# Kernel optimization log

Hardware: AMD Instinct MI355X
Metric: run time of the kernel (lower is better)

The kernel has to match this reference:

```python
import jax, jax.numpy as jnp
import numpy as np

N = 50000
E = 800000
D_IN = 128
D_OUT = 128


def setup_inputs() -> dict:
    key = jax.random.key(0)
    ks = jax.random.split(key, 12)
    x = jax.random.normal(ks[0], (N, D_IN), dtype=jnp.float32)
    W1 = jax.random.normal(ks[1], (D_IN, D_OUT), dtype=jnp.float32) * (1.0 / np.sqrt(D_IN))
    b1 = jnp.zeros((D_OUT,), dtype=jnp.float32)
    W2 = jax.random.normal(ks[2], (D_IN, D_OUT), dtype=jnp.float32) * (1.0 / np.sqrt(D_IN))
    b2 = jnp.zeros((D_OUT,), dtype=jnp.float32)
    # inverted-dropout masks, p=0.5 -> values in {0, 2}
    def mask(k):
        return jnp.where(jax.random.uniform(k, (N, D_IN)) < 0.5, 0.0, 2.0).astype(jnp.float32)
    mask_pos1 = mask(ks[3])
    mask_neg1 = mask(ks[4])
    mask_pos2 = mask(ks[5])
    mask_neg2 = mask(ks[6])
    edge_index1 = jax.random.randint(ks[7], (2, E), 0, N, dtype=jnp.int32)
    edge_index2 = jax.random.randint(ks[8], (2, E), 0, N, dtype=jnp.int32)
    perm1 = jax.random.permutation(ks[9], N).astype(jnp.int32)
    perm2 = jax.random.permutation(ks[10], N).astype(jnp.int32)
    return dict(x=x, W1=W1, b1=b1, W2=W2, b2=b2,
                mask_pos1=mask_pos1, mask_neg1=mask_neg1,
                mask_pos2=mask_pos2, mask_neg2=mask_neg2,
                edge_index1=edge_index1, edge_index2=edge_index2,
                perm1=perm1, perm2=perm2)


def gcn_conv(x, W, b, edge_index):
    """PyG GCNConv: add self-loops, symmetric normalization, then x@W aggregation + bias."""
    n = x.shape[0]
    xw = x @ W  # [N, D_OUT]
    loops = jnp.arange(n, dtype=edge_index.dtype)
    src = jnp.concatenate([edge_index[0], loops])
    dst = jnp.concatenate([edge_index[1], loops])
    deg = jax.ops.segment_sum(jnp.ones_like(dst, dtype=xw.dtype), dst, num_segments=n)
    dinv = jax.lax.rsqrt(jnp.maximum(deg, 1.0))  # deg >= 1 due to self-loops
    norm = dinv[src] * dinv[dst]                 # [E+N]
    msg = xw[src] * norm[:, None]                # [E+N, D_OUT]
    out = jax.ops.segment_sum(msg, dst, num_segments=n)
    return out + b


def _branch(x, W, b, edge_index, mask_pos, mask_neg, perm):
    pos_h = jax.nn.relu(gcn_conv(x * mask_pos, W, b, edge_index))
    neg_in = (x * mask_neg)[perm]
    neg_h = jax.nn.relu(gcn_conv(neg_in, W, b, edge_index))
    summary = jnp.mean(pos_h, axis=0, keepdims=True)  # [1, D_OUT]
    return pos_h, neg_h, summary


def reference(x, W1, b1, W2, b2, mask_pos1, mask_neg1, mask_pos2, mask_neg2,
              edge_index1, edge_index2, perm1, perm2):
    p1, n1, s1 = _branch(x, W1, b1, edge_index1, mask_pos1, mask_neg1, perm1)
    p2, n2, s2 = _branch(x, W2, b2, edge_index2, mask_pos2, mask_neg2, perm2)
    return (p1, n1, s1, p2, n2, s2)
```

## Files before the change

kernel.cpp:

```cpp
#include <hip/hip_runtime.h>
#include <hip/hip_fp16.h>

#define NN 50000
#define NE 800000
#define D 128
#define NB 196
#define FILL_BLOCKS 1024
#define GEMM_BLOCKS 3128
#define RNG 6250
#define ESL 6250

typedef _Float16 half8_t __attribute__((ext_vector_type(8)));
typedef _Float16 half4_t __attribute__((ext_vector_type(4)));
typedef float f32x4 __attribute__((ext_vector_type(4)));

__global__ void k_init(int* cnt1, int* cnt2, float* s1, float* s2) {
    int i = blockIdx.x * blockDim.x + threadIdx.x;
    int stride = gridDim.x * blockDim.x;
    for (int j = i; j < NN; j += stride) { cnt1[j] = 0; cnt2[j] = 0; }
    if (i < D) { s1[i] = 0.f; s2[i] = 0.f; }
}

__global__ void k_count(const int* __restrict__ dst1, const int* __restrict__ dst2,
                        int* cnt1, int* cnt2) {
    int r = blockIdx.x & 7;
    int rank = blockIdx.x >> 3;
    unsigned lo = r * RNG;
    int base = rank * ESL;
    for (int e = base + threadIdx.x; e < base + ESL; e += 256) {
        int d1 = dst1[e];
        if ((unsigned)(d1 - lo) < RNG) atomicAdd(&cnt1[d1], 1);
        int d2 = dst2[e];
        if ((unsigned)(d2 - lo) < RNG) atomicAdd(&cnt2[d2], 1);
    }
}

__global__ void k_part(const int* __restrict__ cnt1, const int* __restrict__ cnt2,
                       int* part1, int* part2) {
    __shared__ int sm1[256], sm2[256];
    int t = threadIdx.x;
    int idx = blockIdx.x * 256 + t;
    int v1 = (idx < NN) ? cnt1[idx] : 0;
    int v2 = (idx < NN) ? cnt2[idx] : 0;
    sm1[t] = v1; sm2[t] = v2;
    __syncthreads();
    for (int off = 128; off > 0; off >>= 1) {
        if (t < off) { sm1[t] += sm1[t + off]; sm2[t] += sm2[t + off]; }
        __syncthreads();
    }
    if (t == 0) { part1[blockIdx.x] = sm1[0]; part2[blockIdx.x] = sm2[0]; }
}

__global__ void k_scanp(int* part1, int* part2) {
    __shared__ int sm1[256], sm2[256];
    int t = threadIdx.x;
    int v1 = (t < NB) ? part1[t] : 0;
    int v2 = (t < NB) ? part2[t] : 0;
    sm1[t] = v1; sm2[t] = v2;
    __syncthreads();
    for (int off = 1; off < 256; off <<= 1) {
        int a1 = (t >= off) ? sm1[t - off] : 0;
        int a2 = (t >= off) ? sm2[t - off] : 0;
        __syncthreads();
        sm1[t] += a1; sm2[t] += a2;
        __syncthreads();
    }
    if (t < NB) { part1[t] = sm1[t] - v1; part2[t] = sm2[t] - v2; }
}

__global__ void k_apply(const int* __restrict__ cnt1, const int* __restrict__ cnt2,
                        const int* __restrict__ part1, const int* __restrict__ part2,
                        int* rp1, int* rp2, int* cur1, int* cur2,
                        float* dinv1, float* dinv2) {
    __shared__ int sm1[256], sm2[256];
    int b = blockIdx.x, t = threadIdx.x;
    int idx = b * 256 + t;
    int v1 = (idx < NN) ? cnt1[idx] : 0;
    int v2 = (idx < NN) ? cnt2[idx] : 0;
    sm1[t] = v1; sm2[t] = v2;
    __syncthreads();
    for (int off = 1; off < 256; off <<= 1) {
        int a1 = (t >= off) ? sm1[t - off] : 0;
        int a2 = (t >= off) ? sm2[t - off] : 0;
        __syncthreads();
        sm1[t] += a1; sm2[t] += a2;
        __syncthreads();
    }
    int e1 = sm1[t] - v1 + part1[b];
    int e2 = sm2[t] - v2 + part2[b];
    if (idx < NN) {
        rp1[idx] = e1; cur1[idx] = e1; dinv1[idx] = rsqrtf((float)(v1 + 1));
        rp2[idx] = e2; cur2[idx] = e2; dinv2[idx] = rsqrtf((float)(v2 + 1));
    } else if (idx == NN) {
        rp1[NN] = e1; rp2[NN] = e2;
    }
}

__launch_bounds__(256)
__global__ void k_fill_gemm(const int* __restrict__ src1, const int* __restrict__ dst1,
                            const int* __restrict__ src2, const int* __restrict__ dst2,
                            int* cur1, int* cur2, int* col1, int* col2,
                            const float* __restrict__ x,
                            const float* __restrict__ W1, const float* __restrict__ W2,
                            const float* __restrict__ mp1, const float* __restrict__ mn1,
                            const float* __restrict__ mp2, const float* __restrict__ mn2,
                            const int* __restrict__ perm1, const int* __restrict__ perm2,
                            const float* __restrict__ dinv1, const float* __restrict__ dinv2,
                            _Float16* xwi1, _Float16* xwi2) {
    __shared__ __align__(16) _Float16 WT[128][136];
    int t = threadIdx.x;
    int bid = blockIdx.x;

    if (bid < FILL_BLOCKS) {
        int r = bid & 7;
        int rank = bid >> 3;
        unsigned lo = r * RNG;
        int base = rank * ESL;
        for (int e = base + t; e < base + ESL; e += 256) {
            int d1 = dst1[e];
            if ((unsigned)(d1 - lo) < RNG) {
                int p = atomicAdd(&cur1[d1], 1);
                col1[p] = src1[e];
            }
            int d2 = dst2[e];
            if ((unsigned)(d2 - lo) < RNG) {
                int p = atomicAdd(&cur2[d2], 1);
                col2[p] = src2[e];
            }
        }
        return;
    }

    int g = bid - FILL_BLOCKS;
    int which = g / 782;
    int bx = g - which * 782;
    const float* W = (which < 2) ? W1 : W2;
    const float* mask = (which == 0) ? mp1 : (which == 1) ? mn1 : (which == 2) ? mp2 : mn2;
    const int* perm = (which == 1) ? perm1 : (which == 3) ? perm2 : nullptr;
    const float* dinv = (which < 2) ? dinv1 : dinv2;
    _Float16* out = ((which < 2) ? xwi1 : xwi2) + ((which & 1) ? 128 : 0);

    #pragma unroll
    for (int i = 0; i < 8; i++) {
        int idx = i * 256 + t;
        int j = idx & 127;
        int k0 = (idx >> 7) * 8;
        half8_t h;
        #pragma unroll
        for (int c = 0; c < 8; c++) h[c] = (_Float16)W[(k0 + c) * 128 + j];
        *(half8_t*)(&WT[j][k0]) = h;
    }
    __syncthreads();

    int wave = t >> 6;
    int lane = t & 63;
    int quad = lane >> 4;
    int m = lane & 15;
    int tile = bx * 4 + wave;
    bool active = (tile * 16 < NN);

    f32x4 accs[8];
    if (active) {
        int row = tile * 16 + m;
        int grow = perm ? perm[row] : row;
        const float* xrow = x + (long)grow * D;
        const float* mrow = mask + (long)grow * D;

        half8_t a[4];
        #pragma unroll
        for (int kk = 0; kk < 4; kk++) {
            int k0 = kk * 32 + quad * 8;
            float4 xa = *(const float4*)(xrow + k0);
            float4 xb = *(const float4*)(xrow + k0 + 4);
            float4 ma = *(const float4*)(mrow + k0);
            float4 mb = *(const float4*)(mrow + k0 + 4);
            a[kk][0] = (_Float16)(xa.x * ma.x);
            a[kk][1] = (_Float16)(xa.y * ma.y);
            a[kk][2] = (_Float16)(xa.z * ma.z);
            a[kk][3] = (_Float16)(xa.w * ma.w);
            a[kk][4] = (_Float16)(xb.x * mb.x);
            a[kk][5] = (_Float16)(xb.y * mb.y);
            a[kk][6] = (_Float16)(xb.z * mb.z);
            a[kk][7] = (_Float16)(xb.w * mb.w);
        }

        #pragma unroll
        for (int nt = 0; nt < 8; nt++) {
            f32x4 acc = {0.f, 0.f, 0.f, 0.f};
            #pragma unroll
            for (int kk = 0; kk < 4; kk++) {
                half8_t w = *(const half8_t*)(&WT[nt * 16 + m][kk * 32 + quad * 8]);
                acc = __builtin_amdgcn_mfma_f32_16x16x32_f16(w, a[kk], acc, 0, 0, 0);
            }
            accs[nt] = acc;
        }
    }

    __syncthreads();

    if (active) {
        float ds = dinv[tile * 16 + m];
        _Float16* st = &WT[0][0] + wave * 2176;

        #pragma unroll
        for (int nt = 0; nt < 8; nt++) {
            half4_t h;
            h[0] = (_Float16)(accs[nt][0] * ds);
            h[1] = (_Float16)(accs[nt][1] * ds);
            h[2] = (_Float16)(accs[nt][2] * ds);
            h[3] = (_Float16)(accs[nt][3] * ds);
            *(half4_t*)(st + m * 136 + nt * 16 + quad * 4) = h;
        }
        #pragma unroll
        for (int p = 0; p < 4; p++) {
            int r = lane & 15;
            int cc = (lane >> 4) + p * 4;
            half8_t v = *(const half8_t*)(st + r * 136 + cc * 8);
            *(half8_t*)(out + (long)(tile * 16 + r) * 256 + cc * 8) = v;
        }
    }
}

__launch_bounds__(256)
__global__ void k_agg(const _Float16* __restrict__ xwi1, const _Float16* __restrict__ xwi2,
                      const int* __restrict__ rp1, const int* __restrict__ col1,
                      const float* __restrict__ dinv1,
                      const int* __restrict__ rp2, const int* __restrict__ col2,
                      const float* __restrict__ dinv2,
                      const float* __restrict__ b1, const float* __restrict__ b2,
                      float* out) {
    int g = blockIdx.y;
    const _Float16* xwi = g ? xwi2 : xwi1;
    const int* rp = g ? rp2 : rp1;
    const int* col = g ? col2 : col1;
    const float* dinv = g ? dinv2 : dinv1;
    const float* bias = g ? b2 : b1;
    float* pos_out = out + (g ? 12800128L : 0L);
    float* neg_out = out + (g ? 19200128L : 6400000L);

    int t = threadIdx.x;
    int wave = t >> 6, lane = t & 63;
    int i = blockIdx.x * 4 + wave;
    if (i >= NN) return;
    int j4 = lane * 4;

    half4_t sv = *(const half4_t*)(xwi + (long)i * 256 + j4);
    float a0 = (float)sv[0], a1 = (float)sv[1], a2 = (float)sv[2], a3 = (float)sv[3];
    int e0 = rp[i], e1 = rp[i + 1];
    int e = e0;
    for (; e + 8 <= e1; e += 8) {
        int s0 = col[e + 0], s1 = col[e + 1], s2 = col[e + 2], s3 = col[e + 3];
        int s4 = col[e + 4], s5 = col[e + 5], s6 = col[e + 6], s7 = col[e + 7];
        half4_t v0 = *(const half4_t*)(xwi + (long)s0 * 256 + j4);
        half4_t v1 = *(const half4_t*)(xwi + (long)s1 * 256 + j4);
        half4_t v2 = *(const half4_t*)(xwi + (long)s2 * 256 + j4);
        half4_t v3 = *(const half4_t*)(xwi + (long)s3 * 256 + j4);
        half4_t v4 = *(const half4_t*)(xwi + (long)s4 * 256 + j4);
        half4_t v5 = *(const half4_t*)(xwi + (long)s5 * 256 + j4);
        half4_t v6 = *(const half4_t*)(xwi + (long)s6 * 256 + j4);
        half4_t v7 = *(const half4_t*)(xwi + (long)s7 * 256 + j4);
        a0 += (float)v0[0] + (float)v1[0] + (float)v2[0] + (float)v3[0]
            + (float)v4[0] + (float)v5[0] + (float)v6[0] + (float)v7[0];
        a1 += (float)v0[1] + (float)v1[1] + (float)v2[1] + (float)v3[1]
            + (float)v4[1] + (float)v5[1] + (float)v6[1] + (float)v7[1];
        a2 += (float)v0[2] + (float)v1[2] + (float)v2[2] + (float)v3[2]
            + (float)v4[2] + (float)v5[2] + (float)v6[2] + (float)v7[2];
        a3 += (float)v0[3] + (float)v1[3] + (float)v2[3] + (float)v3[3]
            + (float)v4[3] + (float)v5[3] + (float)v6[3] + (float)v7[3];
    }
    for (; e + 4 <= e1; e += 4) {
        int s0 = col[e + 0], s1 = col[e + 1], s2 = col[e + 2], s3 = col[e + 3];
        half4_t v0 = *(const half4_t*)(xwi + (long)s0 * 256 + j4);
        half4_t v1 = *(const half4_t*)(xwi + (long)s1 * 256 + j4);
        half4_t v2 = *(const half4_t*)(xwi + (long)s2 * 256 + j4);
        half4_t v3 = *(const half4_t*)(xwi + (long)s3 * 256 + j4);
        a0 += (float)v0[0] + (float)v1[0] + (float)v2[0] + (float)v3[0];
        a1 += (float)v0[1] + (float)v1[1] + (float)v2[1] + (float)v3[1];
        a2 += (float)v0[2] + (float)v1[2] + (float)v2[2] + (float)v3[2];
        a3 += (float)v0[3] + (float)v1[3] + (float)v2[3] + (float)v3[3];
    }
    for (; e < e1; e++) {
        int s = col[e];
        half4_t v = *(const half4_t*)(xwi + (long)s * 256 + j4);
        a0 += (float)v[0]; a1 += (float)v[1]; a2 += (float)v[2]; a3 += (float)v[3];
    }
    float di = dinv[i];
    int jj = (lane < 32) ? j4 : (j4 - 128);
    const f32x4* bp = (const f32x4*)(bias + jj);
    f32x4 bv = *bp;
    f32x4 o;
    o[0] = fmaxf(0.f, di * a0 + bv[0]);
    o[1] = fmaxf(0.f, di * a1 + bv[1]);
    o[2] = fmaxf(0.f, di * a2 + bv[2]);
    o[3] = fmaxf(0.f, di * a3 + bv[3]);
    float* dst = ((lane < 32) ? pos_out : neg_out) + (long)i * D + jj;
    __builtin_nontemporal_store(o, (f32x4*)dst);
}

__launch_bounds__(256)
__global__ void k_sum(const float* __restrict__ pos1, const float* __restrict__ pos2,
                      float* s1, float* s2) {
    int g = blockIdx.y;
    const float* pos = g ? pos2 : pos1;
    float* s = g ? s2 : s1;
    int t = threadIdx.x;
    int rg = t >> 5;
    int j = (t & 31) * 4;
    float4 acc = {0.f, 0.f, 0.f, 0.f};
    for (int i = blockIdx.x * 8 + rg; i < NN; i += gridDim.x * 8) {
        float4 v = *(const float4*)(pos + (long)i * D + j);
        acc.x += v.x; acc.y += v.y; acc.z += v.z; acc.w += v.w;
    }
    __shared__ float sm[8][128];
    sm[rg][j + 0] = acc.x;
    sm[rg][j + 1] = acc.y;
    sm[rg][j + 2] = acc.z;
    sm[rg][j + 3] = acc.w;
    __syncthreads();
    if (t < 128) {
        float v = 0.f;
        for (int r = 0; r < 8; r++) v += sm[r][t];
        atomicAdd(&s[t], v * (1.0f / NN));
    }
}

extern "C" void kernel_launch(void* const* d_in, const int* in_sizes, int n_in,
                              void* d_out, int out_size, void* d_ws, size_t ws_size,
                              hipStream_t stream) {
    const float* x   = (const float*)d_in[0];
    const float* W1  = (const float*)d_in[1];
    const float* b1  = (const float*)d_in[2];
    const float* W2  = (const float*)d_in[3];
    const float* b2  = (const float*)d_in[4];
    const float* mp1 = (const float*)d_in[5];
    const float* mn1 = (const float*)d_in[6];
    const float* mp2 = (const float*)d_in[7];
    const float* mn2 = (const float*)d_in[8];
    const int* e1 = (const int*)d_in[9];
    const int* e2 = (const int*)d_in[10];
    const int* perm1 = (const int*)d_in[11];
    const int* perm2 = (const int*)d_in[12];
    const int* src1 = e1;       const int* dst1 = e1 + NE;
    const int* src2 = e2;       const int* dst2 = e2 + NE;
    float* out = (float*)d_out;

    char* w = (char*)d_ws;
    _Float16* xwi1 = (_Float16*)w; w += (size_t)NN * 256 * 2;
    _Float16* xwi2 = (_Float16*)w; w += (size_t)NN * 256 * 2;
    int* cnt1 = (int*)w;  w += (size_t)NN * 4;
    int* cnt2 = (int*)w;  w += (size_t)NN * 4;
    int* cur1 = (int*)w;  w += (size_t)NN * 4;
    int* cur2 = (int*)w;  w += (size_t)NN * 4;
    int* rp1 = (int*)w;   w += (size_t)(NN + 4) * 4;
    int* rp2 = (int*)w;   w += (size_t)(NN + 4) * 4;
    int* col1 = (int*)w;  w += (size_t)NE * 4;
    int* col2 = (int*)w;  w += (size_t)NE * 4;
    float* dinv1 = (float*)w; w += (size_t)NN * 4;
    float* dinv2 = (float*)w; w += (size_t)NN * 4;
    int* part1 = (int*)w; w += (size_t)256 * 4;
    int* part2 = (int*)w; w += (size_t)256 * 4;

    float* s1 = out + 12800000L;
    float* s2 = out + 25600128L;
    const float* pos1 = out;
    const float* pos2 = out + 12800128L;

    k_init<<<dim3(256), 256, 0, stream>>>(cnt1, cnt2, s1, s2);
    k_count<<<dim3(1024), 256, 0, stream>>>(dst1, dst2, cnt1, cnt2);
    k_part<<<dim3(NB), 256, 0, stream>>>(cnt1, cnt2, part1, part2);
    k_scanp<<<dim3(1), 256, 0, stream>>>(part1, part2);
    k_apply<<<dim3(NB), 256, 0, stream>>>(cnt1, cnt2, part1, part2,
                                          rp1, rp2, cur1, cur2, dinv1, dinv2);
    k_fill_gemm<<<dim3(FILL_BLOCKS + GEMM_BLOCKS), 256, 0, stream>>>(
        src1, dst1, src2, dst2, cur1, cur2, col1, col2,
        x, W1, W2, mp1, mn1, mp2, mn2, perm1, perm2, dinv1, dinv2, xwi1, xwi2);
    k_agg<<<dim3(12500, 2), 256, 0, stream>>>(xwi1, xwi2,
                                              rp1, col1, dinv1, rp2, col2, dinv2,
                                              b1, b2, out);
    k_sum<<<dim3(128, 2), 256, 0, stream>>>(pos1, pos2, s1, s2);
}
```

Measured before the change: 521.1 us.

## Pretranspose weights once and split fused fill/GEMM into separate kernels

The W transpose and fp16 conversion move into k_init, producing a 128x128 half-precision WT buffer per layer in workspace. Previously each of the 3128 GEMM blocks rebuilt it in shared memory. The GEMM kernel now reads W fragments straight from global/L2 and uses only a small per-wave shared staging buffer, which removes the block-level barriers and lowers LDS use. The CSR fill and the GEMM become two sequential launches instead of one fused launch, so the concurrency between the two phases is lost.

```diff
diff --git a/kernel.cpp b/kernel.cpp
--- a/kernel.cpp
+++ b/kernel.cpp
@@ -14,11 +14,18 @@
 typedef _Float16 half4_t __attribute__((ext_vector_type(4)));
 typedef float f32x4 __attribute__((ext_vector_type(4)));
 
-__global__ void k_init(int* cnt1, int* cnt2, float* s1, float* s2) {
+__global__ void k_init(int* cnt1, int* cnt2, float* s1, float* s2,
+                       const float* __restrict__ W1, const float* __restrict__ W2,
+                       _Float16* wt1, _Float16* wt2) {
     int i = blockIdx.x * blockDim.x + threadIdx.x;
     int stride = gridDim.x * blockDim.x;
     for (int j = i; j < NN; j += stride) { cnt1[j] = 0; cnt2[j] = 0; }
     if (i < D) { s1[i] = 0.f; s2[i] = 0.f; }
+    if (i < 16384) {
+        int n = i >> 7, k = i & 127;
+        wt1[n * 128 + k] = (_Float16)W1[k * 128 + n];
+        wt2[n * 128 + k] = (_Float16)W2[k * 128 + n];
+    }
 }
 
 __global__ void k_count(const int* __restrict__ dst1, const int* __restrict__ dst2,
@@ -96,128 +103,108 @@
     }
 }
 
+__global__ void k_fill(const int* __restrict__ src1, const int* __restrict__ dst1,
+                       const int* __restrict__ src2, const int* __restrict__ dst2,
+                       int* cur1, int* cur2, int* col1, int* col2) {
+    int r = blockIdx.x & 7;
+    int rank = blockIdx.x >> 3;
+    unsigned lo = r * RNG;
+    int base = rank * ESL;
+    for (int e = base + threadIdx.x; e < base + ESL; e += 256) {
+        int d1 = dst1[e];
+        if ((unsigned)(d1 - lo) < RNG) {
+            int p = atomicAdd(&cur1[d1], 1);
+            col1[p] = src1[e];
+        }
+        int d2 = dst2[e];
+        if ((unsigned)(d2 - lo) < RNG) {
+            int p = atomicAdd(&cur2[d2], 1);
+            col2[p] = src2[e];
+        }
+    }
+}
+
 __launch_bounds__(256)
-__global__ void k_fill_gemm(const int* __restrict__ src1, const int* __restrict__ dst1,
-                            const int* __restrict__ src2, const int* __restrict__ dst2,
-                            int* cur1, int* cur2, int* col1, int* col2,
-                            const float* __restrict__ x,
-                            const float* __restrict__ W1, const float* __restrict__ W2,
-                            const float* __restrict__ mp1, const float* __restrict__ mn1,
-                            const float* __restrict__ mp2, const float* __restrict__ mn2,
-                            const int* __restrict__ perm1, const int* __restrict__ perm2,
-                            const float* __restrict__ dinv1, const float* __restrict__ dinv2,
-                            _Float16* xwi1, _Float16* xwi2) {
-    __shared__ __align__(16) _Float16 WT[128][136];
-    int t = threadIdx.x;
-    int bid = blockIdx.x;
-
-    if (bid < FILL_BLOCKS) {
-        int r = bid & 7;
-        int rank = bid >> 3;
-        unsigned lo = r * RNG;
-        int base = rank * ESL;
-        for (int e = base + t; e < base + ESL; e += 256) {
-            int d1 = dst1[e];
-            if ((unsigned)(d1 - lo) < RNG) {
-                int p = atomicAdd(&cur1[d1], 1);
-                col1[p] = src1[e];
-            }
-            int d2 = dst2[e];
-            if ((unsigned)(d2 - lo) < RNG) {
-                int p = atomicAdd(&cur2[d2], 1);
-                col2[p] = src2[e];
-            }
-        }
-        return;
-    }
-
-    int g = bid - FILL_BLOCKS;
+__global__ void k_gemm(const _Float16* __restrict__ wt1, const _Float16* __restrict__ wt2,
+                       const float* __restrict__ x,
+                       const float* __restrict__ mp1, const float* __restrict__ mn1,
+                       const float* __restrict__ mp2, const float* __restrict__ mn2,
+                       const int* __restrict__ perm1, const int* __restrict__ perm2,
+                       const float* __restrict__ dinv1, const float* __restrict__ dinv2,
+                       _Float16* xwi1, _Float16* xwi2) {
+    __shared__ __align__(16) _Float16 ST[4][16][136];
+
+    int g = blockIdx.x;
     int which = g / 782;
     int bx = g - which * 782;
-    const float* W = (which < 2) ? W1 : W2;
+    const _Float16* wt = (which < 2) ? wt1 : wt2;
     const float* mask = (which == 0) ? mp1 : (which == 1) ? mn1 : (which == 2) ? mp2 : mn2;
     const int* perm = (which == 1) ? perm1 : (which == 3) ? perm2 : nullptr;
     const float* dinv = (which < 2) ? dinv1 : dinv2;
     _Float16* out = ((which < 2) ? xwi1 : xwi2) + ((which & 1) ? 128 : 0);
 
-    #pragma unroll
-    for (int i = 0; i < 8; i++) {
-        int idx = i * 256 + t;
-        int j = idx & 127;
-        int k0 = (idx >> 7) * 8;
-        half8_t h;
-        #pragma unroll
-        for (int c = 0; c < 8; c++) h[c] = (_Float16)W[(k0 + c) * 128 + j];
-        *(half8_t*)(&WT[j][k0]) = h;
-    }
-    __syncthreads();
-
+    int t = threadIdx.x;
     int wave = t >> 6;
     int lane = t & 63;
     int quad = lane >> 4;
     int m = lane & 15;
     int tile = bx * 4 + wave;
-    bool active = (tile * 16 < NN);
+    if (tile * 16 >= NN) return;
+
+    int row = tile * 16 + m;
+    int grow = perm ? perm[row] : row;
+    const float* xrow = x + (long)grow * D;
+    const float* mrow = mask + (long)grow * D;
+
+    half8_t a[4];
+    #pragma unroll
+    for (int kk = 0; kk < 4; kk++) {
+        int k0 = kk * 32 + quad * 8;
+        float4 xa = *(const float4*)(xrow + k0);
+        float4 xb = *(const float4*)(xrow + k0 + 4);
+        float4 ma = *(const float4*)(mrow + k0);
+        float4 mb = *(const float4*)(mrow + k0 + 4);
+        a[kk][0] = (_Float16)(xa.x * ma.x);
+        a[kk][1] = (_Float16)(xa.y * ma.y);
+        a[kk][2] = (_Float16)(xa.z * ma.z);
+        a[kk][3] = (_Float16)(xa.w * ma.w);
+        a[kk][4] = (_Float16)(xb.x * mb.x);
+        a[kk][5] = (_Float16)(xb.y * mb.y);
+        a[kk][6] = (_Float16)(xb.z * mb.z);
+        a[kk][7] = (_Float16)(xb.w * mb.w);
+    }
 
     f32x4 accs[8];
-    if (active) {
-        int row = tile * 16 + m;
-        int grow = perm ? perm[row] : row;
-        const float* xrow = x + (long)grow * D;
-        const float* mrow = mask + (long)grow * D;
-
-        half8_t a[4];
+    #pragma unroll
+    for (int nt = 0; nt < 8; nt++) {
+        const _Float16* wrow = wt + (nt * 16 + m) * 128 + quad * 8;
+        f32x4 acc = {0.f, 0.f, 0.f, 0.f};
         #pragma unroll
         for (int kk = 0; kk < 4; kk++) {
-            int k0 = kk * 32 + quad * 8;
-            float4 xa = *(const float4*)(xrow + k0);
-            float4 xb = *(const float4*)(xrow + k0 + 4);
-            float4 ma = *(const float4*)(mrow + k0);
-            float4 mb = *(const float4*)(mrow + k0 + 4);
-            a[kk][0] = (_Float16)(xa.x * ma.x);
-            a[kk][1] = (_Float16)(xa.y * ma.y);
-            a[kk][2] = (_Float16)(xa.z * ma.z);
-            a[kk][3] = (_Float16)(xa.w * ma.w);
-            a[kk][4] = (_Float16)(xb.x * mb.x);
-            a[kk][5] = (_Float16)(xb.y * mb.y);
-            a[kk][6] = (_Float16)(xb.z * mb.z);
-            a[kk][7] = (_Float16)(xb.w * mb.w);
+            half8_t w = *(const half8_t*)(wrow + kk * 32);
+            acc = __builtin_amdgcn_mfma_f32_16x16x32_f16(w, a[kk], acc, 0, 0, 0);
         }
-
-        #pragma unroll
-        for (int nt = 0; nt < 8; nt++) {
-            f32x4 acc = {0.f, 0.f, 0.f, 0.f};
-            #pragma unroll
-            for (int kk = 0; kk < 4; kk++) {
-                half8_t w = *(const half8_t*)(&WT[nt * 16 + m][kk * 32 + quad * 8]);
-                acc = __builtin_amdgcn_mfma_f32_16x16x32_f16(w, a[kk], acc, 0, 0, 0);
-            }
-            accs[nt] = acc;
-        }
-    }
-
-    __syncthreads();
-
-    if (active) {
-        float ds = dinv[tile * 16 + m];
-        _Float16* st = &WT[0][0] + wave * 2176;
-
-        #pragma unroll
-        for (int nt = 0; nt < 8; nt++) {
-            half4_t h;
-            h[0] = (_Float16)(accs[nt][0] * ds);
-            h[1] = (_Float16)(accs[nt][1] * ds);
-            h[2] = (_Float16)(accs[nt][2] * ds);
-            h[3] = (_Float16)(accs[nt][3] * ds);
-            *(half4_t*)(st + m * 136 + nt * 16 + quad * 4) = h;
-        }
-        #pragma unroll
-        for (int p = 0; p < 4; p++) {
-            int r = lane & 15;
-            int cc = (lane >> 4) + p * 4;
-            half8_t v = *(const half8_t*)(st + r * 136 + cc * 8);
-            *(half8_t*)(out + (long)(tile * 16 + r) * 256 + cc * 8) = v;
-        }
+        accs[nt] = acc;
+    }
+
+    float ds = dinv[tile * 16 + m];
+    _Float16* st = &ST[wave][0][0];
+
+    #pragma unroll
+    for (int nt = 0; nt < 8; nt++) {
+        half4_t h;
+        h[0] = (_Float16)(accs[nt][0] * ds);
+        h[1] = (_Float16)(accs[nt][1] * ds);
+        h[2] = (_Float16)(accs[nt][2] * ds);
+        h[3] = (_Float16)(accs[nt][3] * ds);
+        *(half4_t*)(st + m * 136 + nt * 16 + quad * 4) = h;
+    }
+    #pragma unroll
+    for (int p = 0; p < 4; p++) {
+        int r = lane & 15;
+        int cc = (lane >> 4) + p * 4;
+        half8_t v = *(const half8_t*)(st + r * 136 + cc * 8);
+        *(half8_t*)(out + (long)(tile * 16 + r) * 256 + cc * 8) = v;
     }
 }
 
@@ -359,21 +346,24 @@
     float* dinv2 = (float*)w; w += (size_t)NN * 4;
     int* part1 = (int*)w; w += (size_t)256 * 4;
     int* part2 = (int*)w; w += (size_t)256 * 4;
+    _Float16* wt1 = (_Float16*)w; w += (size_t)D * D * 2;
+    _Float16* wt2 = (_Float16*)w; w += (size_t)D * D * 2;
 
     float* s1 = out + 12800000L;
     float* s2 = out + 25600128L;
     const float* pos1 = out;
     const float* pos2 = out + 12800128L;
 
-    k_init<<<dim3(256), 256, 0, stream>>>(cnt1, cnt2, s1, s2);
+    k_init<<<dim3(256), 256, 0, stream>>>(cnt1, cnt2, s1, s2, W1, W2, wt1, wt2);
     k_count<<<dim3(1024), 256, 0, stream>>>(dst1, dst2, cnt1, cnt2);
     k_part<<<dim3(NB), 256, 0, stream>>>(cnt1, cnt2, part1, part2);
     k_scanp<<<dim3(1), 256, 0, stream>>>(part1, part2);
     k_apply<<<dim3(NB), 256, 0, stream>>>(cnt1, cnt2, part1, part2,
                                           rp1, rp2, cur1, cur2, dinv1, dinv2);
-    k_fill_gemm<<<dim3(FILL_BLOCKS + GEMM_BLOCKS), 256, 0, stream>>>(
-        src1, dst1, src2, dst2, cur1, cur2, col1, col2,
-        x, W1, W2, mp1, mn1, mp2, mn2, perm1, perm2, dinv1, dinv2, xwi1, xwi2);
+    k_fill<<<dim3(FILL_BLOCKS), 256, 0, stream>>>(src1, dst1, src2, dst2,
+                                                  cur1, cur2, col1, col2);
+    k_gemm<<<dim3(GEMM_BLOCKS), 256, 0, stream>>>(wt1, wt2,
+        x, mp1, mn1, mp2, mn2, perm1, perm2, dinv1, dinv2, xwi1, xwi2);
     k_agg<<<dim3(12500, 2), 256, 0, stream>>>(xwi1, xwi2,
                                               rp1, col1, dinv1, rp2, col2, dinv2,
                                               b1, b2, out);
```

Result: slower. 556.9 us (+6.9%).

## Pre-bucket edges by destination range before counting and CSR fill

Applied to the files above, without the earlier changes.

Adds a bucketing pass that partitions both edge lists into 8 destination-range buckets using shared-memory counters and global offsets. The count and fill kernels then read only their bucket's edges, so they no longer scan all 800K edges eight times with range filtering. This adds an extra kernel launch plus roughly 16MB of scratch writes and reads. The per-bucket capacity BCAP silently drops any edges beyond it, which is safe only because uniform random destinations keep each bucket near 100K.

```diff
diff --git a/kernel.cpp b/kernel.cpp
--- a/kernel.cpp
+++ b/kernel.cpp
@@ -8,31 +8,76 @@
 #define FILL_BLOCKS 1024
 #define GEMM_BLOCKS 3128
 #define RNG 6250
-#define ESL 6250
+#define BCAP 131072
 
 typedef _Float16 half8_t __attribute__((ext_vector_type(8)));
 typedef _Float16 half4_t __attribute__((ext_vector_type(4)));
 typedef float f32x4 __attribute__((ext_vector_type(4)));
 
-__global__ void k_init(int* cnt1, int* cnt2, float* s1, float* s2) {
+__global__ void k_init(int* cnt1, int* cnt2, float* s1, float* s2, int* bcnt) {
     int i = blockIdx.x * blockDim.x + threadIdx.x;
     int stride = gridDim.x * blockDim.x;
     for (int j = i; j < NN; j += stride) { cnt1[j] = 0; cnt2[j] = 0; }
     if (i < D) { s1[i] = 0.f; s2[i] = 0.f; }
-}
-
-__global__ void k_count(const int* __restrict__ dst1, const int* __restrict__ dst2,
-                        int* cnt1, int* cnt2) {
-    int r = blockIdx.x & 7;
+    if (i < 16) bcnt[i] = 0;
+}
+
+__global__ void k_bucket(const int* __restrict__ src1, const int* __restrict__ dst1,
+                         const int* __restrict__ src2, const int* __restrict__ dst2,
+                         int* bcnt,
+                         int* bs1, int* bd1, int* bs2, int* bd2) {
+    __shared__ int lcnt[16], lpos[16], gbase[16];
+    int t = threadIdx.x;
+    if (t < 16) { lcnt[t] = 0; lpos[t] = 0; }
+    __syncthreads();
+
+    int e0 = blockIdx.x * 256 + t;
+    int s1v0=0,d1v0=0,s2v0=0,d2v0=0, s1v1=0,d1v1=0,s2v1=0,d2v1=0;
+    int s1v2=0,d1v2=0,s2v2=0,d2v2=0, s1v3=0,d1v3=0,s2v3=0,d2v3=0;
+    bool v0 = (e0 + 0 * 262144) < NE;
+    bool v1 = (e0 + 1 * 262144) < NE;
+    bool v2 = (e0 + 2 * 262144) < NE;
+    bool v3 = (e0 + 3 * 262144) < NE;
+    if (v0) { int e = e0;             s1v0 = src1[e]; d1v0 = dst1[e]; s2v0 = src2[e]; d2v0 = dst2[e]; }
+    if (v1) { int e = e0 + 262144;    s1v1 = src1[e]; d1v1 = dst1[e]; s2v1 = src2[e]; d2v1 = dst2[e]; }
+    if (v2) { int e = e0 + 2*262144;  s1v2 = src1[e]; d1v2 = dst1[e]; s2v2 = src2[e]; d2v2 = dst2[e]; }
+    if (v3) { int e = e0 + 3*262144;  s1v3 = src1[e]; d1v3 = dst1[e]; s2v3 = src2[e]; d2v3 = dst2[e]; }
+
+    if (v0) { atomicAdd(&lcnt[d1v0 / RNG], 1); atomicAdd(&lcnt[8 + d2v0 / RNG], 1); }
+    if (v1) { atomicAdd(&lcnt[d1v1 / RNG], 1); atomicAdd(&lcnt[8 + d2v1 / RNG], 1); }
+    if (v2) { atomicAdd(&lcnt[d1v2 / RNG], 1); atomicAdd(&lcnt[8 + d2v2 / RNG], 1); }
+    if (v3) { atomicAdd(&lcnt[d1v3 / RNG], 1); atomicAdd(&lcnt[8 + d2v3 / RNG], 1); }
+    __syncthreads();
+    if (t < 16) gbase[t] = atomicAdd(&bcnt[t], lcnt[t]);
+    __syncthreads();
+
+    #define PLACE(sv, dv) { \
+        int r = (dv) / RNG; \
+        int p = gbase[r] + atomicAdd(&lpos[r], 1); \
+        if (p < BCAP) { bs1[r * BCAP + p] = (sv); bd1[r * BCAP + p] = (dv); } }
+    #define PLACE2(sv, dv) { \
+        int r = (dv) / RNG; \
+        int p = gbase[8 + r] + atomicAdd(&lpos[8 + r], 1); \
+        if (p < BCAP) { bs2[r * BCAP + p] = (sv); bd2[r * BCAP + p] = (dv); } }
+    if (v0) { PLACE(s1v0, d1v0); PLACE2(s2v0, d2v0); }
+    if (v1) { PLACE(s1v1, d1v1); PLACE2(s2v1, d2v1); }
+    if (v2) { PLACE(s1v2, d1v2); PLACE2(s2v2, d2v2); }
+    if (v3) { PLACE(s1v3, d1v3); PLACE2(s2v3, d2v3); }
+    #undef PLACE
+    #undef PLACE2
+}
+
+__global__ void k_count_b(const int* __restrict__ bcnt,
+                          const int* __restrict__ bd1, const int* __restrict__ bd2,
+                          int* cnt1, int* cnt2) {
+    int b = blockIdx.x & 7;
     int rank = blockIdx.x >> 3;
-    unsigned lo = r * RNG;
-    int base = rank * ESL;
-    for (int e = base + threadIdx.x; e < base + ESL; e += 256) {
-        int d1 = dst1[e];
-        if ((unsigned)(d1 - lo) < RNG) atomicAdd(&cnt1[d1], 1);
-        int d2 = dst2[e];
-        if ((unsigned)(d2 - lo) < RNG) atomicAdd(&cnt2[d2], 1);
-    }
+    int base = b * BCAP;
+    int n1 = bcnt[b], n2 = bcnt[8 + b];
+    for (int i = rank * 256 + threadIdx.x; i < n1; i += 32768)
+        atomicAdd(&cnt1[bd1[base + i]], 1);
+    for (int i = rank * 256 + threadIdx.x; i < n2; i += 32768)
+        atomicAdd(&cnt2[bd2[base + i]], 1);
 }
 
 __global__ void k_part(const int* __restrict__ cnt1, const int* __restrict__ cnt2,
@@ -97,8 +142,9 @@
 }
 
 __launch_bounds__(256)
-__global__ void k_fill_gemm(const int* __restrict__ src1, const int* __restrict__ dst1,
-                            const int* __restrict__ src2, const int* __restrict__ dst2,
+__global__ void k_fill_gemm(const int* __restrict__ bcnt,
+                            const int* __restrict__ bs1, const int* __restrict__ bd1,
+                            const int* __restrict__ bs2, const int* __restrict__ bd2,
                             int* cur1, int* cur2, int* col1, int* col2,
                             const float* __restrict__ x,
                             const float* __restrict__ W1, const float* __restrict__ W2,
@@ -112,21 +158,19 @@
     int bid = blockIdx.x;
 
     if (bid < FILL_BLOCKS) {
-        int r = bid & 7;
+        int b = bid & 7;
         int rank = bid >> 3;
-        unsigned lo = r * RNG;
-        int base = rank * ESL;
-        for (int e = base + t; e < base + ESL; e += 256) {
-            int d1 = dst1[e];
-            if ((unsigned)(d1 - lo) < RNG) {
-                int p = atomicAdd(&cur1[d1], 1);
-                col1[p] = src1[e];
-            }
-            int d2 = dst2[e];
-            if ((unsigned)(d2 - lo) < RNG) {
-                int p = atomicAdd(&cur2[d2], 1);
-                col2[p] = src2[e];
-            }
+        int base = b * BCAP;
+        int n1 = bcnt[b], n2 = bcnt[8 + b];
+        for (int i = rank * 256 + t; i < n1; i += 32768) {
+            int d = bd1[base + i];
+            int p = atomicAdd(&cur1[d], 1);
+            col1[p] = bs1[base + i];
+        }
+        for (int i = rank * 256 + t; i < n2; i += 32768) {
+            int d = bd2[base + i];
+            int p = atomicAdd(&cur2[d], 1);
+            col2[p] = bs2[base + i];
         }
         return;
     }
@@ -359,20 +403,27 @@
     float* dinv2 = (float*)w; w += (size_t)NN * 4;
     int* part1 = (int*)w; w += (size_t)256 * 4;
     int* part2 = (int*)w; w += (size_t)256 * 4;
+    int* bcnt  = (int*)w; w += (size_t)64 * 4;
+    int* bs1 = (int*)w;   w += (size_t)8 * BCAP * 4;
+    int* bd1 = (int*)w;   w += (size_t)8 * BCAP * 4;
+    int* bs2 = (int*)w;   w += (size_t)8 * BCAP * 4;
+    int* bd2 = (int*)w;   w += (size_t)8 * BCAP * 4;
 
     float* s1 = out + 12800000L;
     float* s2 = out + 25600128L;
     const float* pos1 = out;
     const float* pos2 = out + 12800128L;
 
-    k_init<<<dim3(256), 256, 0, stream>>>(cnt1, cnt2, s1, s2);
-    k_count<<<dim3(1024), 256, 0, stream>>>(dst1, dst2, cnt1, cnt2);
+    k_init<<<dim3(256), 256, 0, stream>>>(cnt1, cnt2, s1, s2, bcnt);
+    k_bucket<<<dim3(1024), 256, 0, stream>>>(src1, dst1, src2, dst2, bcnt,
+                                             bs1, bd1, bs2, bd2);
+    k_count_b<<<dim3(1024), 256, 0, stream>>>(bcnt, bd1, bd2, cnt1, cnt2);
     k_part<<<dim3(NB), 256, 0, stream>>>(cnt1, cnt2, part1, part2);
     k_scanp<<<dim3(1), 256, 0, stream>>>(part1, part2);
     k_apply<<<dim3(NB), 256, 0, stream>>>(cnt1, cnt2, part1, part2,
                                           rp1, rp2, cur1, cur2, dinv1, dinv2);
     k_fill_gemm<<<dim3(FILL_BLOCKS + GEMM_BLOCKS), 256, 0, stream>>>(
-        src1, dst1, src2, dst2, cur1, cur2, col1, col2,
+        bcnt, bs1, bd1, bs2, bd2, cur1, cur2, col1, col2,
         x, W1, W2, mp1, mn1, mp2, mn2, perm1, perm2, dinv1, dinv2, xwi1, xwi2);
     k_agg<<<dim3(12500, 2), 256, 0, stream>>>(xwi1, xwi2,
                                               rp1, col1, dinv1, rp2, col2, dinv2,
```

Result: no change. 529.6 us (+1.6%).
